# Kernel tuning notes

Measured on AMD Instinct MI355X. Metric: run time of the kernel, lower is better.

## Reference

```python
import jax, jax.numpy as jnp
import numpy as np


def setup_inputs() -> dict:
    key = jax.random.key(0)
    k1, k2, k3, k4 = jax.random.split(key, 4)
    N, Ck, Cv, T, H, W = 8, 128, 512, 8, 30, 30
    return {
        "q_key": jax.random.normal(k1, (N, Ck, H, W), dtype=jnp.float32),
        "q_val": jax.random.normal(k2, (N, Cv, H, W), dtype=jnp.float32),
        "m_key": jax.random.normal(k3, (N, Ck, T, H, W), dtype=jnp.float32),
        "m_val": jax.random.normal(k4, (N, Cv, T, H, W), dtype=jnp.float32),
    }


def reference(q_key, q_val, m_key, m_val):
    N, Ck, H, W = q_key.shape
    _, Cv, T, Hm, Wm = m_val.shape
    qk = q_key.reshape(N, Ck, H * W)            # n c q
    mk = m_key.reshape(N, Ck, T * Hm * Wm)      # n c m
    # affinity [n, q, m], scaled by 1/sqrt(Ck)
    aff = jnp.einsum("ncq,ncm->nqm", qk, mk) * (Ck ** -0.5)
    # NOTE: softmax over the QUERY axis (axis=1), per the original module
    attn = jax.nn.softmax(aff, axis=1)
    mv = m_val.reshape(N, Cv, T * Hm * Wm)      # n c m
    mapped = jnp.einsum("nqm,ncm->ncq", attn, mv).reshape(N, Cv, Hm, Wm)
    return jnp.concatenate([q_val, mapped], axis=1)  # [N, 2*Cv, H, W]
```

## Files before the change

kernel.cpp:

```cpp
#include <hip/hip_runtime.h>
#include <stdint.h>

#define N_  8
#define CK  128
#define CV  512
#define HW  900
#define M_  7200
#define QK_SCALE 0.08838834764831845f

typedef __attribute__((ext_vector_type(8))) short  short8;
typedef __attribute__((ext_vector_type(4))) float  floatx4;
typedef __attribute__((ext_vector_type(4))) unsigned int   uintx4;
typedef __attribute__((ext_vector_type(4))) unsigned short ushortx4;

__device__ __forceinline__ uint16_t f32_to_bf16(float x) {
    union { float f; uint32_t u; } v; v.f = x;
    return (uint16_t)((v.u + 0x7FFFu + ((v.u >> 16) & 1u)) >> 16);
}

__device__ __forceinline__ void gload_lds16(const uint16_t* g, short* l) {
    __builtin_amdgcn_global_load_lds(
        (const __attribute__((address_space(1))) void*)g,
        (__attribute__((address_space(3))) void*)l,
        16, 0, 0);
}

__global__ void k_zero(float* __restrict__ p) {
    int i = blockIdx.x * 256 + threadIdx.x;
    if (i < N_ * M_) p[i] = 0.f;
}

__global__ __launch_bounds__(256) void k_copy_qval(const float* __restrict__ qv,
                                                   float* __restrict__ out) {
    unsigned i = blockIdx.x * 256 + threadIdx.x;
    unsigned e = i * 4u;
    unsigned n = e / (CV * HW);
    unsigned off = e - n * (CV * HW);
    *(floatx4*)&out[(size_t)n * (2 * CV * HW) + off] = *(const floatx4*)&qv[e];
}

__global__ __launch_bounds__(256) void k_trans(const float* __restrict__ in,
                                               uint16_t* __restrict__ outp, int L) {
    __shared__ float tile[32][33];
    const int tx = threadIdx.x & 31;
    const int ty = threadIdx.x >> 5;
    const int l0 = blockIdx.x * 32;
    const int c0 = blockIdx.y * 32;
    const int n  = blockIdx.z;
    const float* src = in + (size_t)n * CK * L;
    uint16_t* dst = outp + (size_t)n * L * CK;
#pragma unroll
    for (int p = 0; p < 4; p++) {
        int c = c0 + p * 8 + ty;
        int l = l0 + tx;
        float v = 0.f;
        if (l < L) v = src[(size_t)c * L + l];
        tile[p * 8 + ty][tx] = v;
    }
    __syncthreads();
#pragma unroll
    for (int p = 0; p < 4; p++) {
        int l = l0 + p * 8 + ty;
        int c = c0 + tx;
        if (l < L) dst[(size_t)l * CK + c] = f32_to_bf16(tile[tx][p * 8 + ty]);
    }
}

#define K1_TS 144

__global__ __launch_bounds__(256) void k1_gemm_exp(
    const uint16_t* __restrict__ qkT,
    const uint16_t* __restrict__ mkT,
    uint16_t* __restrict__ E,
    float* __restrict__ dsum)
{
    __shared__ __align__(16) short smem[18432];
    __shared__ float colsum[128];

    const int bid = blockIdx.x + 57 * (blockIdx.y + 8 * blockIdx.z);
    const int swz = (bid & 7) * 456 + (bid >> 3);
    const int mb   = swz % 57;
    const int rest = swz / 57;
    const int m0 = mb * 128;
    const int q0 = (rest & 7) * 128;
    const int n  = rest >> 3;
    const int tid = threadIdx.x;

    if (tid < 128) colsum[tid] = 0.f;

    const int lane = tid & 63;
    const int wid  = tid >> 6;
    const int wq   = (wid >> 1) << 6;
    const int wm   = (wid & 1) << 6;
    const int fr   = lane & 15;
    const int quad = lane >> 4;

    const int ca = wid * 2;
    const int rr = lane >> 2;
    const int cc = (lane & 3) * 8;

    const uint16_t* Ab = qkT + (size_t)n * HW * CK;
    const uint16_t* Bb = mkT + (size_t)n * M_ * CK;
    const uint16_t* A0p = Ab + (size_t)(q0 + ca * 16 + rr) * CK + cc;
    const uint16_t* A1p = A0p + 16 * CK;
    const uint16_t* B0p = Bb + (size_t)(m0 + ca * 16 + rr) * CK + cc;
    const uint16_t* B1p = B0p + 16 * CK;

    floatx4 acc[4][4];
#pragma unroll
    for (int a = 0; a < 4; a++)
#pragma unroll
        for (int b = 0; b < 4; b++) acc[a][b] = (floatx4){0.f, 0.f, 0.f, 0.f};

#define K1_STAGE(buf, ko) do { \
    gload_lds16(A0p + (ko), smem + (buf) * 4096 + ca * 512); \
    gload_lds16(A1p + (ko), smem + (buf) * 4096 + ca * 512 + 512); \
    gload_lds16(B0p + (ko), smem + 8192 + (buf) * 4096 + ca * 512); \
    gload_lds16(B1p + (ko), smem + 8192 + (buf) * 4096 + ca * 512 + 512); \
} while (0)

#define K1_COMPUTE(buf) do { \
    const int k0 = quad * 8; \
    short8 af[4], bfr[4]; \
    _Pragma("unroll") \
    for (int t = 0; t < 4; t++) \
        af[t] = *(const short8*)&smem[(buf) * 4096 + (wq + t * 16 + fr) * 32 + k0]; \
    _Pragma("unroll") \
    for (int t = 0; t < 4; t++) \
        bfr[t] = *(const short8*)&smem[8192 + (buf) * 4096 + (wm + t * 16 + fr) * 32 + k0]; \
    _Pragma("unroll") \
    for (int tq = 0; tq < 4; tq++) \
        _Pragma("unroll") \
        for (int tm = 0; tm < 4; tm++) \
            acc[tq][tm] = __builtin_amdgcn_mfma_f32_16x16x32_bf16( \
                af[tq], bfr[tm], acc[tq][tm], 0, 0, 0); \
} while (0)

    K1_STAGE(0, 0);
    __syncthreads();
    K1_STAGE(1, 32); K1_COMPUTE(0); __syncthreads();
    K1_STAGE(0, 64); K1_COMPUTE(1); __syncthreads();
    K1_STAGE(1, 96); K1_COMPUTE(0); __syncthreads();
    K1_COMPUTE(1);

    __syncthreads();
    float cs[4] = {0.f, 0.f, 0.f, 0.f};
#pragma unroll
    for (int tq = 0; tq < 4; tq++) {
#pragma unroll
        for (int tm = 0; tm < 4; tm++) {
            const int col = wm + tm * 16 + fr;
#pragma unroll
            for (int i = 0; i < 4; i++) {
                const int row = wq + tq * 16 + quad * 4 + i;
                float e = __expf(acc[tq][tm][i] * QK_SCALE);
                if (q0 + row < HW) cs[tm] += e;
                smem[row * K1_TS + col] = (short)f32_to_bf16(e);
            }
        }
    }
#pragma unroll
    for (int tm = 0; tm < 4; tm++) {
        float s = cs[tm];
        s += __shfl_xor(s, 16, 64);
        s += __shfl_xor(s, 32, 64);
        if (quad == 0) atomicAdd(&colsum[wm + tm * 16 + fr], s);
    }
    __syncthreads();

    uint16_t* En = E + (size_t)n * HW * M_;
#pragma unroll
    for (int j = 0; j < 8; j++) {
        int idx = tid + j * 256;
        int r   = idx >> 4;
        int c8  = (idx & 15) * 8;
        if (q0 + r < HW && m0 + c8 + 8 <= M_) {
            uintx4 v = *(const uintx4*)&smem[r * K1_TS + c8];
            *(uintx4*)&En[(size_t)(q0 + r) * M_ + m0 + c8] = v;
        }
    }
    if (tid < 128) {
        const int gm = m0 + tid;
        if (gm < M_) atomicAdd(&dsum[(size_t)n * M_ + gm], colsum[tid]);
    }
#undef K1_STAGE
#undef K1_COMPUTE
}

__global__ void k_dinv(const float* __restrict__ d, float* __restrict__ di) {
    int i = blockIdx.x * 256 + threadIdx.x;
    if (i < N_ * M_) di[i] = 1.0f / d[i];
}

__global__ __launch_bounds__(256) void k_mvs(
    const float* __restrict__ mval,
    const float* __restrict__ dinv,
    uint16_t* __restrict__ mvs)
{
    unsigned i = blockIdx.x * 256 + threadIdx.x;
    unsigned base = i * 4u;
    unsigned n = base / (unsigned)(CV * M_);
    unsigned m = base % (unsigned)M_;
    floatx4 v  = *(const floatx4*)&mval[base];
    floatx4 di = *(const floatx4*)&dinv[n * (unsigned)M_ + m];
    ushortx4 o;
    o[0] = f32_to_bf16(v[0] * di[0]);
    o[1] = f32_to_bf16(v[1] * di[1]);
    o[2] = f32_to_bf16(v[2] * di[2]);
    o[3] = f32_to_bf16(v[3] * di[3]);
    *(ushortx4*)&mvs[base] = o;
}

#define K2_SPLITS 3
#define K2_BK 32
#define K2_STEPS 75

__global__ __launch_bounds__(256) void k2_split3(
    const uint16_t* __restrict__ mvs,
    const uint16_t* __restrict__ E,
    float* __restrict__ partials)
{
    __shared__ __align__(16) short lds2[16384];

    const int bid = blockIdx.x + 8 * (blockIdx.y + 4 * blockIdx.z);
    const int swz = (bid & 7) * 96 + (bid >> 3);
    const int q0 = (swz & 7) << 7;
    const int c0 = ((swz >> 3) & 3) << 7;
    const int nz = swz >> 5;
    const int n     = nz / K2_SPLITS;
    const int split = nz - n * K2_SPLITS;
    const int tid = threadIdx.x;

    const int lane = tid & 63;
    const int wid  = tid >> 6;
    const int wc   = (wid >> 1) << 6;
    const int wq   = (wid & 1) << 6;
    const int fr   = lane & 15;
    const int quad = lane >> 4;

    const int ca = wid * 2;
    const int rr = lane >> 2;
    const int cc = (lane & 3) * 8;

    const uint16_t* Asrc = mvs + (size_t)(n * CV + c0) * M_ + split * 2400;
    const uint16_t* Bsrc = E + (size_t)n * HW * M_ + split * 2400;
    const uint16_t* A0p = Asrc + (size_t)(ca * 16 + rr) * M_ + cc;
    const uint16_t* A1p = A0p + (size_t)16 * M_;
    const uint16_t* B0p = Bsrc + (size_t)(q0 + ca * 16 + rr) * M_ + cc;
    const uint16_t* B1p = B0p + (size_t)16 * M_;

    floatx4 acc[4][4];
#pragma unroll
    for (int a = 0; a < 4; a++)
#pragma unroll
        for (int b = 0; b < 4; b++) acc[a][b] = (floatx4){0.f, 0.f, 0.f, 0.f};

#define K2_STAGE(buf, mo) do { \
    gload_lds16(A0p + (mo), lds2 + (buf) * 4096 + ca * 512); \
    gload_lds16(A1p + (mo), lds2 + (buf) * 4096 + ca * 512 + 512); \
    gload_lds16(B0p + (mo), lds2 + 8192 + (buf) * 4096 + ca * 512); \
    gload_lds16(B1p + (mo), lds2 + 8192 + (buf) * 4096 + ca * 512 + 512); \
} while (0)

#define K2_COMPUTE(buf) do { \
    const int k0 = quad * 8; \
    short8 af[4], bfr[4]; \
    _Pragma("unroll") \
    for (int t = 0; t < 4; t++) \
        af[t] = *(const short8*)&lds2[(buf) * 4096 + (wc + t * 16 + fr) * 32 + k0]; \
    _Pragma("unroll") \
    for (int t = 0; t < 4; t++) \
        bfr[t] = *(const short8*)&lds2[8192 + (buf) * 4096 + (wq + t * 16 + fr) * 32 + k0]; \
    _Pragma("unroll") \
    for (int tc = 0; tc < 4; tc++) \
        _Pragma("unroll") \
        for (int tq = 0; tq < 4; tq++) \
            acc[tc][tq] = __builtin_amdgcn_mfma_f32_16x16x32_bf16( \
                af[tc], bfr[tq], acc[tc][tq], 0, 0, 0); \
} while (0)

    K2_STAGE(0, 0);
    __syncthreads();
    for (int s = 0; s < K2_STEPS - 1; s += 2) {
        K2_STAGE(1, (s + 1) * K2_BK);
        K2_COMPUTE(0);
        __syncthreads();
        K2_STAGE(0, (s + 2) * K2_BK);
        K2_COMPUTE(1);
        __syncthreads();
    }
    K2_COMPUTE(0);

    float* P = partials + ((size_t)split * N_ + n) * CV * HW;
#pragma unroll
    for (int tc = 0; tc < 4; tc++) {
#pragma unroll
        for (int tq = 0; tq < 4; tq++) {
            const int gq = q0 + wq + tq * 16 + fr;
            if (gq < HW) {
#pragma unroll
                for (int i = 0; i < 4; i++) {
                    const int gc = c0 + wc + tc * 16 + quad * 4 + i;
                    P[(size_t)gc * HW + gq] = acc[tc][tq][i];
                }
            }
        }
    }
#undef K2_STAGE
#undef K2_COMPUTE
}

__global__ __launch_bounds__(256) void k_reduce3(const float* __restrict__ partials,
                                                 float* __restrict__ out) {
    unsigned i = blockIdx.x * 256 + threadIdx.x;
    unsigned e = i * 4u;
    unsigned n = e / (CV * HW);
    unsigned off = e - n * (CV * HW);
    const size_t stride = (size_t)N_ * CV * HW;
    const float* p = partials + (size_t)n * CV * HW + off;
    floatx4 a = *(const floatx4*)&p[0];
    floatx4 b = *(const floatx4*)&p[stride];
    floatx4 c = *(const floatx4*)&p[2 * stride];
    floatx4 s = a + b + c;
    *(floatx4*)&out[(size_t)n * (2 * CV * HW) + CV * HW + off] = s;
}

extern "C" void kernel_launch(void* const* d_in, const int* in_sizes, int n_in,
                              void* d_out, int out_size, void* d_ws, size_t ws_size,
                              hipStream_t stream) {
    const float* qkey = (const float*)d_in[0];
    const float* qval = (const float*)d_in[1];
    const float* mkey = (const float*)d_in[2];
    const float* mval = (const float*)d_in[3];
    float* out = (float*)d_out;

    char* ws = (char*)d_ws;
    uint16_t* E        = (uint16_t*)ws;
    float*    dsum     = (float*)(ws + 103680000);
    float*    dinv     = (float*)(ws + 103910400);
    uint16_t* mvs      = (uint16_t*)(ws + 104140800);
    float*    partials = (float*)(ws + 163123200);
    uint16_t* qkT      = (uint16_t*)(ws + 163123200);
    uint16_t* mkT      = (uint16_t*)(ws + 163123200 + 1843200);

    (void)in_sizes; (void)n_in; (void)out_size; (void)ws_size;

    k_zero<<<dim3((N_ * M_ + 255) / 256), 256, 0, stream>>>(dsum);
    k_copy_qval<<<dim3((N_ * CV * HW) / 4 / 256), 256, 0, stream>>>(qval, out);
    k_trans<<<dim3(29, 4, N_), 256, 0, stream>>>(qkey, qkT, HW);
    k_trans<<<dim3(225, 4, N_), 256, 0, stream>>>(mkey, mkT, M_);
    k1_gemm_exp<<<dim3(57, 8, N_), 256, 0, stream>>>(qkT, mkT, E, dsum);
    k_dinv<<<dim3((N_ * M_ + 255) / 256), 256, 0, stream>>>(dsum, dinv);
    k_mvs<<<dim3((N_ * CV * M_) / 4 / 256), 256, 0, stream>>>(mval, dinv, mvs);
    k2_split3<<<dim3(8, 4, N_ * K2_SPLITS), 256, 0, stream>>>(mvs, E, partials);
    k_reduce3<<<dim3((N_ * CV * HW) / 4 / 256), 256, 0, stream>>>(partials, out);
}
```

Measured before the change: 419.4 us.

## Deepen both GEMM kernels to a 4-stage LDS ring with vmcnt-gated barriers

Replaces the double-buffered LDS staging in the QK-exp GEMM and the split-K AV GEMM with a four-buffer ring, keeping up to three global→LDS loads in flight. Each step now waits with an explicit s_waitcnt vmcnt and a single raw barrier wrapped in sched_barriers, instead of a full __syncthreads. The aim is to hide global-load latency behind MFMA work. In exchange, LDS per block doubles to 64KB, which can reduce the number of resident blocks per CU.

```diff
diff --git a/kernel.cpp b/kernel.cpp
--- a/kernel.cpp
+++ b/kernel.cpp
@@ -24,6 +24,11 @@
         (__attribute__((address_space(3))) void*)l,
         16, 0, 0);
 }
+
+#define WAITV(n) asm volatile("s_waitcnt vmcnt(" #n ")" ::: "memory")
+#define BARRIER() do { __builtin_amdgcn_sched_barrier(0); \
+                       __builtin_amdgcn_s_barrier(); \
+                       __builtin_amdgcn_sched_barrier(0); } while (0)
 
 __global__ void k_zero(float* __restrict__ p) {
     int i = blockIdx.x * 256 + threadIdx.x;
@@ -74,7 +79,7 @@
     uint16_t* __restrict__ E,
     float* __restrict__ dsum)
 {
-    __shared__ __align__(16) short smem[18432];
+    __shared__ __align__(16) short smem[32768];
     __shared__ float colsum[128];
 
     const int bid = blockIdx.x + 57 * (blockIdx.y + 8 * blockIdx.z);
@@ -113,21 +118,25 @@
         for (int b = 0; b < 4; b++) acc[a][b] = (floatx4){0.f, 0.f, 0.f, 0.f};
 
 #define K1_STAGE(buf, ko) do { \
-    gload_lds16(A0p + (ko), smem + (buf) * 4096 + ca * 512); \
-    gload_lds16(A1p + (ko), smem + (buf) * 4096 + ca * 512 + 512); \
-    gload_lds16(B0p + (ko), smem + 8192 + (buf) * 4096 + ca * 512); \
-    gload_lds16(B1p + (ko), smem + 8192 + (buf) * 4096 + ca * 512 + 512); \
+    short* dA = smem + (buf) * 8192 + ca * 512; \
+    short* dB = dA + 4096; \
+    gload_lds16(A0p + (ko), dA); \
+    gload_lds16(A1p + (ko), dA + 512); \
+    gload_lds16(B0p + (ko), dB); \
+    gload_lds16(B1p + (ko), dB + 512); \
 } while (0)
 
 #define K1_COMPUTE(buf) do { \
+    const short* bA = smem + (buf) * 8192; \
+    const short* bB = bA + 4096; \
     const int k0 = quad * 8; \
     short8 af[4], bfr[4]; \
     _Pragma("unroll") \
     for (int t = 0; t < 4; t++) \
-        af[t] = *(const short8*)&smem[(buf) * 4096 + (wq + t * 16 + fr) * 32 + k0]; \
+        af[t] = *(const short8*)&bA[(wq + t * 16 + fr) * 32 + k0]; \
     _Pragma("unroll") \
     for (int t = 0; t < 4; t++) \
-        bfr[t] = *(const short8*)&smem[8192 + (buf) * 4096 + (wm + t * 16 + fr) * 32 + k0]; \
+        bfr[t] = *(const short8*)&bB[(wm + t * 16 + fr) * 32 + k0]; \
     _Pragma("unroll") \
     for (int tq = 0; tq < 4; tq++) \
         _Pragma("unroll") \
@@ -136,12 +145,11 @@
                 af[tq], bfr[tm], acc[tq][tm], 0, 0, 0); \
 } while (0)
 
-    K1_STAGE(0, 0);
-    __syncthreads();
-    K1_STAGE(1, 32); K1_COMPUTE(0); __syncthreads();
-    K1_STAGE(0, 64); K1_COMPUTE(1); __syncthreads();
-    K1_STAGE(1, 96); K1_COMPUTE(0); __syncthreads();
-    K1_COMPUTE(1);
+    K1_STAGE(0, 0); K1_STAGE(1, 32); K1_STAGE(2, 64);
+    WAITV(8); BARRIER(); K1_STAGE(3, 96); K1_COMPUTE(0);
+    WAITV(8); BARRIER(); K1_COMPUTE(1);
+    WAITV(4); BARRIER(); K1_COMPUTE(2);
+    WAITV(0); BARRIER(); K1_COMPUTE(3);
 
     __syncthreads();
     float cs[4] = {0.f, 0.f, 0.f, 0.f};
@@ -220,7 +228,7 @@
     const uint16_t* __restrict__ E,
     float* __restrict__ partials)
 {
-    __shared__ __align__(16) short lds2[16384];
+    __shared__ __align__(16) short lds2[32768];
 
     const int bid = blockIdx.x + 8 * (blockIdx.y + 4 * blockIdx.z);
     const int swz = (bid & 7) * 96 + (bid >> 3);
@@ -256,21 +264,25 @@
         for (int b = 0; b < 4; b++) acc[a][b] = (floatx4){0.f, 0.f, 0.f, 0.f};
 
 #define K2_STAGE(buf, mo) do { \
-    gload_lds16(A0p + (mo), lds2 + (buf) * 4096 + ca * 512); \
-    gload_lds16(A1p + (mo), lds2 + (buf) * 4096 + ca * 512 + 512); \
-    gload_lds16(B0p + (mo), lds2 + 8192 + (buf) * 4096 + ca * 512); \
-    gload_lds16(B1p + (mo), lds2 + 8192 + (buf) * 4096 + ca * 512 + 512); \
+    short* dA = lds2 + (buf) * 8192 + ca * 512; \
+    short* dB = dA + 4096; \
+    gload_lds16(A0p + (mo), dA); \
+    gload_lds16(A1p + (mo), dA + 512); \
+    gload_lds16(B0p + (mo), dB); \
+    gload_lds16(B1p + (mo), dB + 512); \
 } while (0)
 
 #define K2_COMPUTE(buf) do { \
+    const short* bA = lds2 + (buf) * 8192; \
+    const short* bB = bA + 4096; \
     const int k0 = quad * 8; \
     short8 af[4], bfr[4]; \
     _Pragma("unroll") \
     for (int t = 0; t < 4; t++) \
-        af[t] = *(const short8*)&lds2[(buf) * 4096 + (wc + t * 16 + fr) * 32 + k0]; \
+        af[t] = *(const short8*)&bA[(wc + t * 16 + fr) * 32 + k0]; \
     _Pragma("unroll") \
     for (int t = 0; t < 4; t++) \
-        bfr[t] = *(const short8*)&lds2[8192 + (buf) * 4096 + (wq + t * 16 + fr) * 32 + k0]; \
+        bfr[t] = *(const short8*)&bB[(wq + t * 16 + fr) * 32 + k0]; \
     _Pragma("unroll") \
     for (int tc = 0; tc < 4; tc++) \
         _Pragma("unroll") \
@@ -280,16 +292,16 @@
 } while (0)
 
     K2_STAGE(0, 0);
-    __syncthreads();
-    for (int s = 0; s < K2_STEPS - 1; s += 2) {
-        K2_STAGE(1, (s + 1) * K2_BK);
-        K2_COMPUTE(0);
-        __syncthreads();
-        K2_STAGE(0, (s + 2) * K2_BK);
-        K2_COMPUTE(1);
-        __syncthreads();
-    }
-    K2_COMPUTE(0);
+    K2_STAGE(1, K2_BK);
+    K2_STAGE(2, 2 * K2_BK);
+    for (int t = 0; t < K2_STEPS - 3; ++t) {
+        WAITV(8); BARRIER();
+        K2_STAGE((t + 3) & 3, (t + 3) * K2_BK);
+        K2_COMPUTE(t & 3);
+    }
+    WAITV(8); BARRIER(); K2_COMPUTE(0);
+    WAITV(4); BARRIER(); K2_COMPUTE(1);
+    WAITV(0); BARRIER(); K2_COMPUTE(2);
 
     float* P = partials + ((size_t)split * N_ + n) * CV * HW;
 #pragma unroll
```

Result: no change. 414.8 us (-1.1%).
